# Kernel tuning notes

Measured on AMD Instinct MI355X. Metric: run time of the kernel, lower is better.

## Reference

```python
import jax, jax.numpy as jnp
import numpy as np

N = 50000      # nodes
E = 800000     # edges (avg degree 16)
D = 128        # input feature dim
H = 128        # hidden dim
G = 64         # graphs in batch


def setup_inputs() -> dict:
    key = jax.random.key(0)
    k = jax.random.split(key, 6)
    x = jax.random.normal(k[0], (N, D), dtype=jnp.float32)
    edge_index = jax.random.randint(k[1], (2, E), 0, N, dtype=jnp.int64)
    batch = jnp.sort(jax.random.randint(k[2], (N,), 0, G, dtype=jnp.int64))
    s1 = 1.0 / np.sqrt(D)
    s2 = 1.0 / np.sqrt(H)
    W1 = jax.random.uniform(k[3], (D, H), jnp.float32, -s1, s1)
    b1 = jnp.zeros((H,), jnp.float32)
    W2 = jax.random.uniform(k[4], (H, H), jnp.float32, -s2, s2)
    b2 = jnp.zeros((H,), jnp.float32)
    return {"x": x, "edge_index": edge_index, "batch": batch,
            "W1": W1, "b1": b1, "W2": W2, "b2": b2}


def _gcn_conv(x, src, dst, W, b, n):
    """GCNConv: out = D^{-1/2}(A+I)D^{-1/2} X W + b (self-loops already in src/dst)."""
    h = x @ W                                                   # [n, H]
    deg = jax.ops.segment_sum(jnp.ones(src.shape[0], h.dtype), dst, num_segments=n)
    dinv = jnp.where(deg > 0, jax.lax.rsqrt(deg), 0.0)          # deg^{-1/2}
    norm = dinv[src] * dinv[dst]                                # [E+n]
    out = jax.ops.segment_sum(h[src] * norm[:, None], dst, num_segments=n)
    return out + b


def reference(x, edge_index, batch, W1, b1, W2, b2):
    loop = jnp.arange(N, dtype=edge_index.dtype)
    src = jnp.concatenate([edge_index[0], loop])   # add self-loops
    dst = jnp.concatenate([edge_index[1], loop])
    h = jax.nn.relu(_gcn_conv(x, src, dst, W1, b1, N))
    h = _gcn_conv(h, src, dst, W2, b2, N)          # no activation after last conv
    cnt = jax.ops.segment_sum(jnp.ones(N, h.dtype), batch, num_segments=G)
    pooled = jax.ops.segment_sum(h, batch, num_segments=G) / jnp.maximum(cnt, 1.0)[:, None]
    return pooled  # [G, H]
```

## Files before the change

### kernel.cpp

```cpp
#include <hip/hip_runtime.h>
#include <hip/hip_bf16.h>

#define NN 50000
#define EE 800000
#define HH 128
#define GG 64

#define NB 196
#define CHUNK 4096
#define NBLK ((EE + CHUNK - 1) / CHUNK)
#define CAP 8192
#define PCH 128

typedef __attribute__((ext_vector_type(8))) short short8;
typedef __attribute__((ext_vector_type(4))) float f32x4;

__device__ __forceinline__ unsigned short f2bf(float f) {
    unsigned u = __float_as_uint(f);
    return (unsigned short)((u + 0x7FFFu + ((u >> 16) & 1u)) >> 16);
}
__device__ __forceinline__ float bflo(unsigned p) { return __uint_as_float(p << 16); }
__device__ __forceinline__ float bfhi(unsigned p) { return __uint_as_float(p & 0xFFFF0000u); }
__device__ __forceinline__ float bfu(unsigned short u) { return __uint_as_float(((unsigned)u) << 16); }

#define OFF_BHIST   0
#define OFF_POOLED  (OFF_BHIST + NB*4)
#define ZERO_BYTES  (OFF_POOLED + GG*HH*4)
#define OFF_CURSOR  (ZERO_BYTES)
#define OFF_BOFF    (OFF_CURSOR + NB*4)
#define OFF_GSTART  (OFF_BOFF + (NB+1)*4)
#define OFF_CSROFF  (((OFF_GSTART + (GG+1)*4) + 15)/16*16)
#define OFF_DINV    (((OFF_CSROFF + (NN+1)*4) + 15)/16*16)
#define OFF_WT1     (((OFF_DINV + NN*4) + 15)/16*16)
#define OFF_WT2     (OFF_WT1 + HH*HH*2)
#define OFF_KEYA    (OFF_WT2 + HH*HH*2)
#define OFF_KEYB    (OFF_KEYA + EE*4)
#define OFF_H       (OFF_KEYB + EE*4)
#define OFF_G       (OFF_H + NN*HH*2)


__global__ __launch_bounds__(256) void k1_hist(
    const int* __restrict__ ei, int* __restrict__ bhist)
{
    __shared__ int h[NB];
    int tid = threadIdx.x;
    for (int j = tid; j < NB; j += 256) h[j] = 0;
    __syncthreads();
    int base = blockIdx.x * CHUNK;
    int end = min(base + CHUNK, EE);
    for (int i = base + tid; i < end; i += 256)
        atomicAdd(&h[ei[EE + i] >> 8], 1);
    __syncthreads();
    for (int j = tid; j < NB; j += 256)
        if (h[j]) atomicAdd(&bhist[j], h[j]);
}

__global__ __launch_bounds__(256) void k2_scan(
    const int* __restrict__ bhist, int* __restrict__ boff, int* __restrict__ cursor)
{
    __shared__ int v[NB + 1];
    int tid = threadIdx.x;
    if (tid < NB) v[tid] = bhist[tid];
    __syncthreads();
    if (tid == 0) {
        int run = 0;
        for (int j = 0; j < NB; ++j) { int t = v[j]; v[j] = run; run += t; }
        v[NB] = run;
    }
    __syncthreads();
    if (tid < NB) { boff[tid] = v[tid]; cursor[tid] = v[tid]; }
    if (tid == NB) boff[NB] = v[NB];
}

__global__ __launch_bounds__(256) void k3_scatter(
    const int* __restrict__ ei, int* __restrict__ cursor, unsigned* __restrict__ keyA)
{
    __shared__ int h[NB];
    __shared__ int basev[NB];
    __shared__ int c[NB];
    int tid = threadIdx.x;
    for (int j = tid; j < NB; j += 256) { h[j] = 0; c[j] = 0; }
    __syncthreads();
    int base = blockIdx.x * CHUNK;
    int end = min(base + CHUNK, EE);
    for (int i = base + tid; i < end; i += 256)
        atomicAdd(&h[ei[EE + i] >> 8], 1);
    __syncthreads();
    for (int j = tid; j < NB; j += 256)
        if (h[j]) basev[j] = atomicAdd(&cursor[j], h[j]);
    __syncthreads();
    for (int i = base + tid; i < end; i += 256) {
        int s = ei[i];
        int d = ei[EE + i];
        int b = d >> 8;
        int r = atomicAdd(&c[b], 1);
        keyA[basev[b] + r] = ((unsigned)d << 16) | (unsigned)s;
    }
}

__global__ __launch_bounds__(256) void k4_sort(
    const unsigned* __restrict__ keyA, const int* __restrict__ boff,
    unsigned* __restrict__ keyB, int* __restrict__ csr_off, float* __restrict__ dinv)
{
    __shared__ unsigned keys[CAP];
    __shared__ int h[256];
    __shared__ int off[256];
    int b = blockIdx.x, tid = threadIdx.x;
    int e0 = boff[b], e1 = boff[b + 1], n = e1 - e0;
    h[tid] = 0;
    __syncthreads();
    for (int i = tid; i < n; i += 256) {
        unsigned k = keyA[e0 + i];
        if (i < CAP) keys[i] = k;
        atomicAdd(&h[(k >> 16) & 255], 1);
    }
    __syncthreads();
    if (tid == 0) {
        int run = 0;
        for (int j = 0; j < 256; ++j) { int t = h[j]; off[j] = run; run += t; }
    }
    __syncthreads();
    int d = (b << 8) + tid;
    if (d < NN) {
        csr_off[d] = e0 + off[tid];
        dinv[d] = rsqrtf((float)(h[tid] + 1));
    }
    if (b == 0 && tid == 0) csr_off[NN] = EE;
    __syncthreads();
    h[tid] = 0;
    __syncthreads();
    for (int i = tid; i < n; i += 256) {
        unsigned k = (i < CAP) ? keys[i] : keyA[e0 + i];
        int lo = (k >> 16) & 255;
        int r = atomicAdd(&h[lo], 1);
        keyB[e0 + off[lo] + r] = k;
    }
}

__global__ __launch_bounds__(128) void gstart_kernel(
    const int* __restrict__ batch, int* __restrict__ gstart)
{
    int g = threadIdx.x;
    if (g > GG) return;
    int lo = 0, hi = NN;
    while (lo < hi) {
        int mid = (lo + hi) >> 1;
        if (batch[mid] < g) lo = mid + 1; else hi = mid;
    }
    gstart[g] = lo;
}

__global__ __launch_bounds__(256) void wcast_kernel(
    const float* __restrict__ W1, const float* __restrict__ W2,
    unsigned short* __restrict__ Wt1, unsigned short* __restrict__ Wt2)
{
    int i = blockIdx.x * 256 + threadIdx.x;
    if (i < HH * HH) {
        int r = i >> 7, c = i & 127;
        Wt1[c * HH + r] = f2bf(W1[i]);
        Wt2[c * HH + r] = f2bf(W2[i]);
    }
}

template<bool F32SRC>
__global__ __launch_bounds__(256) void gemm_mfma_kernel(
    const void* __restrict__ Asrc, const unsigned short* __restrict__ Wt,
    const float* __restrict__ dinv, unsigned short* __restrict__ C)
{
    int tid = threadIdx.x;
    int w  = tid >> 6;
    int l  = tid & 63;
    int lr = l & 15;
    int lg = l >> 4;

    short8 bfrag[2][4];
    #pragma unroll
    for (int nt = 0; nt < 2; ++nt)
        #pragma unroll
        for (int kt = 0; kt < 4; ++kt) {
            int n = w * 32 + nt * 16 + lr;
            int k = kt * 32 + lg * 8;
            bfrag[nt][kt] = *(const short8*)(Wt + (size_t)n * HH + k);
        }

    int base0 = blockIdx.x * 64;
    #pragma unroll
    for (int mt = 0; mt < 4; ++mt) {
        int rowA = base0 + mt * 16 + lr;
        short8 afrag[4];
        #pragma unroll
        for (int kt = 0; kt < 4; ++kt) {
            short8 v = {0, 0, 0, 0, 0, 0, 0, 0};
            if (rowA < NN) {
                if (F32SRC) {
                    const float* p = (const float*)Asrc + (size_t)rowA * HH + kt * 32 + lg * 8;
                    f32x4 u0 = *(const f32x4*)p;
                    f32x4 u1 = *(const f32x4*)(p + 4);
                    #pragma unroll
                    for (int j = 0; j < 4; ++j) {
                        v[j]     = (short)f2bf(u0[j]);
                        v[j + 4] = (short)f2bf(u1[j]);
                    }
                } else {
                    v = *(const short8*)((const unsigned short*)Asrc +
                                         (size_t)rowA * HH + kt * 32 + lg * 8);
                }
            }
            afrag[kt] = v;
        }
        f32x4 acc0 = {0.f, 0.f, 0.f, 0.f};
        f32x4 acc1 = {0.f, 0.f, 0.f, 0.f};
        #pragma unroll
        for (int kt = 0; kt < 4; ++kt) {
            acc0 = __builtin_amdgcn_mfma_f32_16x16x32_bf16(afrag[kt], bfrag[0][kt], acc0, 0, 0, 0);
            acc1 = __builtin_amdgcn_mfma_f32_16x16x32_bf16(afrag[kt], bfrag[1][kt], acc1, 0, 0, 0);
        }
        #pragma unroll
        for (int r = 0; r < 4; ++r) {
            int row = base0 + mt * 16 + lg * 4 + r;
            if (row < NN) {
                float dn = dinv[row];
                C[(size_t)row * HH + w * 32 + lr]      = f2bf(acc0[r] * dn);
                C[(size_t)row * HH + w * 32 + 16 + lr] = f2bf(acc1[r] * dn);
            }
        }
    }
}

template<bool FIN>
__global__ __launch_bounds__(256) void agg_kernel(
    const unsigned* __restrict__ hp, const unsigned* __restrict__ keyB,
    const int* __restrict__ csr_off, const float* __restrict__ dinv,
    const float* __restrict__ bias, unsigned* __restrict__ out)
{
    int node = blockIdx.x * 4 + (threadIdx.x >> 6);
    if (node >= NN) return;
    int lane = threadIdx.x & 63;
    float dn = dinv[node];
    unsigned hv = hp[(size_t)node * 64 + lane];
    float ax = bflo(hv), ay = bfhi(hv);
    int e = csr_off[node], e1 = csr_off[node + 1];
    for (; e + 8 <= e1; e += 8) {
        int s0 = keyB[e]     & 0xFFFF;
        int s1 = keyB[e + 1] & 0xFFFF;
        int s2 = keyB[e + 2] & 0xFFFF;
        int s3 = keyB[e + 3] & 0xFFFF;
        int s4 = keyB[e + 4] & 0xFFFF;
        int s5 = keyB[e + 5] & 0xFFFF;
        int s6 = keyB[e + 6] & 0xFFFF;
        int s7 = keyB[e + 7] & 0xFFFF;
        unsigned v0 = hp[(size_t)s0 * 64 + lane];
        unsigned v1 = hp[(size_t)s1 * 64 + lane];
        unsigned v2 = hp[(size_t)s2 * 64 + lane];
        unsigned v3 = hp[(size_t)s3 * 64 + lane];
        unsigned v4 = hp[(size_t)s4 * 64 + lane];
        unsigned v5 = hp[(size_t)s5 * 64 + lane];
        unsigned v6 = hp[(size_t)s6 * 64 + lane];
        unsigned v7 = hp[(size_t)s7 * 64 + lane];
        ax += (bflo(v0) + bflo(v1)) + (bflo(v2) + bflo(v3))
            + (bflo(v4) + bflo(v5)) + (bflo(v6) + bflo(v7));
        ay += (bfhi(v0) + bfhi(v1)) + (bfhi(v2) + bfhi(v3))
            + (bfhi(v4) + bfhi(v5)) + (bfhi(v6) + bfhi(v7));
    }
    for (; e < e1; ++e) {
        int s = keyB[e] & 0xFFFF;
        unsigned v = hp[(size_t)s * 64 + lane];
        ax += bflo(v);
        ay += bfhi(v);
    }
    float ox = ax * dn, oy = ay * dn;
    if (FIN) {
        ox = fmaxf(ox + bias[lane * 2],     0.f);
        oy = fmaxf(oy + bias[lane * 2 + 1], 0.f);
    }
    out[(size_t)node * 64 + lane] = (unsigned)f2bf(ox) | ((unsigned)f2bf(oy) << 16);
}

__global__ __launch_bounds__(128) void pool_partial_kernel(
    const unsigned short* __restrict__ h3, const int* __restrict__ batch,
    float* __restrict__ pooled)
{
    int n0 = blockIdx.x * PCH;
    int n1 = min(n0 + PCH, NN);
    int f = threadIdx.x;
    float acc = 0.f;
    int cur = batch[n0];
    for (int n = n0; n < n1; ++n) {
        int g = batch[n];
        if (g != cur) {
            atomicAdd(&pooled[(size_t)cur * HH + f], acc);
            acc = 0.f;
            cur = g;
        }
        acc += bfu(h3[(size_t)n * HH + f]);
    }
    atomicAdd(&pooled[(size_t)cur * HH + f], acc);
}

__global__ __launch_bounds__(256) void finalize_kernel(
    const float* __restrict__ pooled, const int* __restrict__ gstart,
    const float* __restrict__ b2, float* __restrict__ out)
{
    int i = blockIdx.x * 256 + threadIdx.x;
    if (i < GG * HH) {
        int g = i >> 7;
        int f = i & 127;
        float cnt = (float)(gstart[g + 1] - gstart[g]);
        out[i] = (pooled[i] + cnt * b2[f]) / fmaxf(cnt, 1.f);
    }
}


extern "C" void kernel_launch(void* const* d_in, const int* in_sizes, int n_in,
                              void* d_out, int out_size, void* d_ws, size_t ws_size,
                              hipStream_t stream)
{
    const float* x     = (const float*)d_in[0];
    const int*   ei    = (const int*)d_in[1];
    const int*   batch = (const int*)d_in[2];
    const float* W1    = (const float*)d_in[3];
    const float* b1    = (const float*)d_in[4];
    const float* W2    = (const float*)d_in[5];
    const float* b2    = (const float*)d_in[6];
    float* out = (float*)d_out;

    char* ws = (char*)d_ws;
    int*            bhist   = (int*)(ws + OFF_BHIST);
    float*          pooled  = (float*)(ws + OFF_POOLED);
    int*            cursor  = (int*)(ws + OFF_CURSOR);
    int*            boff    = (int*)(ws + OFF_BOFF);
    int*            gstart  = (int*)(ws + OFF_GSTART);
    int*            csr_off = (int*)(ws + OFF_CSROFF);
    float*          dinv    = (float*)(ws + OFF_DINV);
    unsigned short* Wt1     = (unsigned short*)(ws + OFF_WT1);
    unsigned short* Wt2     = (unsigned short*)(ws + OFF_WT2);
    unsigned*       keyA    = (unsigned*)(ws + OFF_KEYA);
    unsigned*       keyB    = (unsigned*)(ws + OFF_KEYB);
    unsigned short* hbuf    = (unsigned short*)(ws + OFF_H);
    unsigned short* gbuf    = (unsigned short*)(ws + OFF_G);

    hipMemsetAsync(ws, 0, ZERO_BYTES, stream);

    k1_hist<<<NBLK, 256, 0, stream>>>(ei, bhist);
    k2_scan<<<1, 256, 0, stream>>>(bhist, boff, cursor);
    k3_scatter<<<NBLK, 256, 0, stream>>>(ei, cursor, keyA);
    k4_sort<<<NB, 256, 0, stream>>>(keyA, boff, keyB, csr_off, dinv);

    gstart_kernel<<<1, 128, 0, stream>>>(batch, gstart);
    wcast_kernel<<<(HH * HH + 255) / 256, 256, 0, stream>>>(W1, W2, Wt1, Wt2);

    gemm_mfma_kernel<true><<<(NN + 63) / 64, 256, 0, stream>>>(x, Wt1, dinv, hbuf);
    agg_kernel<true><<<(NN + 3) / 4, 256, 0, stream>>>(
        (const unsigned*)hbuf, keyB, csr_off, dinv, b1, (unsigned*)gbuf);

    gemm_mfma_kernel<false><<<(NN + 63) / 64, 256, 0, stream>>>(gbuf, Wt2, dinv, hbuf);
    agg_kernel<false><<<(NN + 3) / 4, 256, 0, stream>>>(
        (const unsigned*)hbuf, keyB, csr_off, dinv, b2, (unsigned*)gbuf);

    pool_partial_kernel<<<(NN + PCH - 1) / PCH, 128, 0, stream>>>(gbuf, batch, pooled);
    finalize_kernel<<<(GG * HH + 255) / 256, 256, 0, stream>>>(pooled, gstart, b2, out);
}
```

Before: 293.7 us.

## Split aggregation into feature-slice passes and fuse mean pooling into second aggregation

The edge aggregation now runs as four passes, each covering a 32-feature slice (64 bytes per row), with 16 nodes per block and 16 lanes per node, so each pass's gather working set is a quarter of the feature table and is more likely to stay in cache. The second aggregation accumulates pooled sums directly through shared-memory and global atomics, which removes the separate pooling kernel and the write and re-read of the final node features. In exchange there are more kernel launches, the edge indices are read four times, and each gather is narrower (64 bytes per row instead of 256). Nodes with uneven degree inside a wavefront also leave lanes idle.

```diff
diff --git a/kernel.cpp b/kernel.cpp
--- a/kernel.cpp
+++ b/kernel.cpp
@@ -10,7 +10,8 @@
 #define CHUNK 4096
 #define NBLK ((EE + CHUNK - 1) / CHUNK)
 #define CAP 8192
-#define PCH 128
+#define NPB 16
+#define AGG_GRID ((NN + NPB - 1) / NPB)
 
 typedef __attribute__((ext_vector_type(8))) short short8;
 typedef __attribute__((ext_vector_type(4))) float f32x4;
@@ -21,7 +22,6 @@
 }
 __device__ __forceinline__ float bflo(unsigned p) { return __uint_as_float(p << 16); }
 __device__ __forceinline__ float bfhi(unsigned p) { return __uint_as_float(p & 0xFFFF0000u); }
-__device__ __forceinline__ float bfu(unsigned short u) { return __uint_as_float(((unsigned)u) << 16); }
 
 #define OFF_BHIST   0
 #define OFF_POOLED  (OFF_BHIST + NB*4)
@@ -227,74 +227,99 @@
     }
 }
 
-template<bool FIN>
-__global__ __launch_bounds__(256) void agg_kernel(
+__global__ __launch_bounds__(256) void agg1_pass_kernel(
     const unsigned* __restrict__ hp, const unsigned* __restrict__ keyB,
     const int* __restrict__ csr_off, const float* __restrict__ dinv,
-    const float* __restrict__ bias, unsigned* __restrict__ out)
-{
-    int node = blockIdx.x * 4 + (threadIdx.x >> 6);
-    if (node >= NN) return;
-    int lane = threadIdx.x & 63;
-    float dn = dinv[node];
-    unsigned hv = hp[(size_t)node * 64 + lane];
-    float ax = bflo(hv), ay = bfhi(hv);
-    int e = csr_off[node], e1 = csr_off[node + 1];
-    for (; e + 8 <= e1; e += 8) {
-        int s0 = keyB[e]     & 0xFFFF;
-        int s1 = keyB[e + 1] & 0xFFFF;
-        int s2 = keyB[e + 2] & 0xFFFF;
-        int s3 = keyB[e + 3] & 0xFFFF;
-        int s4 = keyB[e + 4] & 0xFFFF;
-        int s5 = keyB[e + 5] & 0xFFFF;
-        int s6 = keyB[e + 6] & 0xFFFF;
-        int s7 = keyB[e + 7] & 0xFFFF;
-        unsigned v0 = hp[(size_t)s0 * 64 + lane];
-        unsigned v1 = hp[(size_t)s1 * 64 + lane];
-        unsigned v2 = hp[(size_t)s2 * 64 + lane];
-        unsigned v3 = hp[(size_t)s3 * 64 + lane];
-        unsigned v4 = hp[(size_t)s4 * 64 + lane];
-        unsigned v5 = hp[(size_t)s5 * 64 + lane];
-        unsigned v6 = hp[(size_t)s6 * 64 + lane];
-        unsigned v7 = hp[(size_t)s7 * 64 + lane];
-        ax += (bflo(v0) + bflo(v1)) + (bflo(v2) + bflo(v3))
-            + (bflo(v4) + bflo(v5)) + (bflo(v6) + bflo(v7));
-        ay += (bfhi(v0) + bfhi(v1)) + (bfhi(v2) + bfhi(v3))
-            + (bfhi(v4) + bfhi(v5)) + (bfhi(v6) + bfhi(v7));
-    }
-    for (; e < e1; ++e) {
-        int s = keyB[e] & 0xFFFF;
-        unsigned v = hp[(size_t)s * 64 + lane];
-        ax += bflo(v);
-        ay += bfhi(v);
-    }
-    float ox = ax * dn, oy = ay * dn;
-    if (FIN) {
-        ox = fmaxf(ox + bias[lane * 2],     0.f);
-        oy = fmaxf(oy + bias[lane * 2 + 1], 0.f);
-    }
-    out[(size_t)node * 64 + lane] = (unsigned)f2bf(ox) | ((unsigned)f2bf(oy) << 16);
-}
-
-__global__ __launch_bounds__(128) void pool_partial_kernel(
-    const unsigned short* __restrict__ h3, const int* __restrict__ batch,
-    float* __restrict__ pooled)
-{
-    int n0 = blockIdx.x * PCH;
-    int n1 = min(n0 + PCH, NN);
-    int f = threadIdx.x;
-    float acc = 0.f;
-    int cur = batch[n0];
-    for (int n = n0; n < n1; ++n) {
-        int g = batch[n];
-        if (g != cur) {
-            atomicAdd(&pooled[(size_t)cur * HH + f], acc);
-            acc = 0.f;
-            cur = g;
-        }
-        acc += bfu(h3[(size_t)n * HH + f]);
-    }
-    atomicAdd(&pooled[(size_t)cur * HH + f], acc);
+    const float* __restrict__ bias, unsigned* __restrict__ out, int pass)
+{
+    int tid = threadIdx.x;
+    int q  = tid >> 4;
+    int fl = tid & 15;
+    int node = (int)blockIdx.x * NPB + q;
+    bool nv = node < NN;
+    int nn = nv ? node : NN - 1;
+    float dn = dinv[nn];
+    int e  = nv ? csr_off[nn]     : 0;
+    int e1 = nv ? csr_off[nn + 1] : 0;
+    size_t rowoff = (size_t)(pass << 4) + fl;
+    unsigned hv = hp[(size_t)nn * 64 + rowoff];
+    float a0 = nv ? bflo(hv) : 0.f;
+    float a1 = nv ? bfhi(hv) : 0.f;
+    while (__any(e < e1)) {
+        #pragma unroll
+        for (int j = 0; j < 8; ++j) {
+            bool act = (e + j) < e1;
+            unsigned key = __builtin_nontemporal_load(&keyB[act ? (e + j) : 0]);
+            int s = act ? (int)(key & 0xFFFF) : nn;
+            unsigned v = hp[(size_t)s * 64 + rowoff];
+            if (act) { a0 += bflo(v); a1 += bfhi(v); }
+        }
+        e += 8;
+    }
+    if (nv) {
+        int f = (pass << 5) + (fl << 1);
+        float o0 = fmaxf(a0 * dn + bias[f],     0.f);
+        float o1 = fmaxf(a1 * dn + bias[f + 1], 0.f);
+        unsigned po = (unsigned)f2bf(o0) | ((unsigned)f2bf(o1) << 16);
+        __builtin_nontemporal_store(po, &out[(size_t)nn * 64 + rowoff]);
+    }
+}
+
+__global__ __launch_bounds__(256) void agg2_pool_pass_kernel(
+    const unsigned* __restrict__ hp, const unsigned* __restrict__ keyB,
+    const int* __restrict__ csr_off, const float* __restrict__ dinv,
+    const int* __restrict__ batch, float* __restrict__ pooled, int pass)
+{
+    __shared__ float pp[2][32];
+    int tid = threadIdx.x;
+    if (tid < 64) ((float*)pp)[tid] = 0.f;
+    __syncthreads();
+    int q  = tid >> 4;
+    int fl = tid & 15;
+    int node = (int)blockIdx.x * NPB + q;
+    bool nv = node < NN;
+    int nn = nv ? node : NN - 1;
+    int b0idx = (int)blockIdx.x * NPB;
+    if (b0idx > NN - 1) b0idx = NN - 1;
+    int g0 = batch[b0idx];
+    int gn = batch[nn];
+    float dn = dinv[nn];
+    int e  = nv ? csr_off[nn]     : 0;
+    int e1 = nv ? csr_off[nn + 1] : 0;
+    size_t rowoff = (size_t)(pass << 4) + fl;
+    unsigned hv = hp[(size_t)nn * 64 + rowoff];
+    float a0 = nv ? bflo(hv) : 0.f;
+    float a1 = nv ? bfhi(hv) : 0.f;
+    while (__any(e < e1)) {
+        #pragma unroll
+        for (int j = 0; j < 8; ++j) {
+            bool act = (e + j) < e1;
+            unsigned key = __builtin_nontemporal_load(&keyB[act ? (e + j) : 0]);
+            int s = act ? (int)(key & 0xFFFF) : nn;
+            unsigned v = hp[(size_t)s * 64 + rowoff];
+            if (act) { a0 += bflo(v); a1 += bfhi(v); }
+        }
+        e += 8;
+    }
+    if (nv) {
+        float o0 = a0 * dn, o1 = a1 * dn;
+        int slot = gn - g0;
+        if (slot <= 1) {
+            atomicAdd(&pp[slot][fl * 2],     o0);
+            atomicAdd(&pp[slot][fl * 2 + 1], o1);
+        } else {
+            atomicAdd(&pooled[(size_t)gn * HH + (pass << 5) + fl * 2],     o0);
+            atomicAdd(&pooled[(size_t)gn * HH + (pass << 5) + fl * 2 + 1], o1);
+        }
+    }
+    __syncthreads();
+    if (tid < 32) {
+        float v = pp[0][tid];
+        if (v != 0.f) atomicAdd(&pooled[(size_t)g0 * HH + (pass << 5) + tid], v);
+    } else if (tid < 64) {
+        float v = pp[1][tid - 32];
+        if (v != 0.f) atomicAdd(&pooled[(size_t)(g0 + 1) * HH + (pass << 5) + tid - 32], v);
+    }
 }
 
 __global__ __launch_bounds__(256) void finalize_kernel(
@@ -339,7 +364,7 @@
     unsigned short* hbuf    = (unsigned short*)(ws + OFF_H);
     unsigned short* gbuf    = (unsigned short*)(ws + OFF_G);
 
-    hipMemsetAsync(ws, 0, ZERO_BYTES, stream);
+    (void)hipMemsetAsync(ws, 0, ZERO_BYTES, stream);
 
     k1_hist<<<NBLK, 256, 0, stream>>>(ei, bhist);
     k2_scan<<<1, 256, 0, stream>>>(bhist, boff, cursor);
@@ -350,13 +375,14 @@
     wcast_kernel<<<(HH * HH + 255) / 256, 256, 0, stream>>>(W1, W2, Wt1, Wt2);
 
     gemm_mfma_kernel<true><<<(NN + 63) / 64, 256, 0, stream>>>(x, Wt1, dinv, hbuf);
-    agg_kernel<true><<<(NN + 3) / 4, 256, 0, stream>>>(
-        (const unsigned*)hbuf, keyB, csr_off, dinv, b1, (unsigned*)gbuf);
+    for (int p = 0; p < 4; ++p)
+        agg1_pass_kernel<<<AGG_GRID, 256, 0, stream>>>(
+            (const unsigned*)hbuf, keyB, csr_off, dinv, b1, (unsigned*)gbuf, p);
 
     gemm_mfma_kernel<false><<<(NN + 63) / 64, 256, 0, stream>>>(gbuf, Wt2, dinv, hbuf);
-    agg_kernel<false><<<(NN + 3) / 4, 256, 0, stream>>>(
-        (const unsigned*)hbuf, keyB, csr_off, dinv, b2, (unsigned*)gbuf);
-
-    pool_partial_kernel<<<(NN + PCH - 1) / PCH, 128, 0, stream>>>(gbuf, batch, pooled);
+    for (int p = 0; p < 4; ++p)
+        agg2_pool_pass_kernel<<<AGG_GRID, 256, 0, stream>>>(
+            (const unsigned*)hbuf, keyB, csr_off, dinv, batch, pooled, p);
+
     finalize_kernel<<<(GG * HH + 255) / 256, 256, 0, stream>>>(pooled, gstart, b2, out);
 }
```

After: 520.3 us. 1.77x slower.
